# Kernel optimization log

Measured on AMD Instinct MI355X. Metric: run time of the kernel, lower is better.

Reference implementation:

```python
import jax, jax.numpy as jnp
import numpy as np

D = 512  # input_channels
K = 64   # centers_num


def setup_inputs() -> dict:
    key = jax.random.key(0)
    k1, k2, k3, k4 = jax.random.split(key, 4)
    inputs = jax.random.normal(k1, (32, D, 56, 56), dtype=jnp.float32)
    # conv 1x1 weight/bias (nn.Conv2d(input_channels, centers_num, (1,1)))
    conv_w = jax.random.normal(k2, (K, D), dtype=jnp.float32) * (1.0 / np.sqrt(D))
    conv_b = jax.random.normal(k3, (K,), dtype=jnp.float32) * 0.01
    # centers ~ U(-0.1, 0.1), shape [D, K]
    centers = jax.random.uniform(k4, (D, K), dtype=jnp.float32, minval=-0.1, maxval=0.1)
    return {"inputs": inputs, "conv_w": conv_w, "conv_b": conv_b, "centers": centers}


def reference(inputs, conv_w, conv_b, centers):
    B, d, H, W = inputs.shape
    N = H * W
    x = inputs.reshape(B, d, N)                      # [B,D,N]
    # 1x1 conv == per-pixel linear: logits [B,K,N]
    logits = jnp.einsum('kd,bdn->bkn', conv_w, x) + conv_b[None, :, None]
    alpha = jax.nn.softmax(logits, axis=1)           # softmax over K (dim=1)
    # vlad[b,d,k] = sum_n alpha[b,k,n] * (x[b,d,n] - centers[d,k])
    vlad = jnp.einsum('bkn,bdn->bdk', alpha, x) - centers[None] * alpha.sum(axis=2)[:, None, :]
    # intra-normalize over D (torch.norm default p=2, no eps)
    vlad = vlad / jnp.linalg.norm(vlad, axis=1, keepdims=True)
    vlad = vlad.reshape(B, d * K)
    vlad = vlad / jnp.linalg.norm(vlad, axis=1, keepdims=True)
    return vlad
```

## Files before the change

### kernel.cpp

```cpp
#include <hip/hip_runtime.h>
#include <math.h>


#define NN 3136
#define DD 512
#define KK 64
#define BB 32

typedef short bf16x8 __attribute__((ext_vector_type(8)));
typedef float f32x4  __attribute__((ext_vector_type(4)));

#define SEL_HI   0x05040100u
#define SEL_LO   0x07060302u
#define SEL_PACK 0x07060302u

union FragU { uint4 u; bf16x8 f; };

static __device__ inline bf16x8 frag4(unsigned a, unsigned b, unsigned c, unsigned d) {
    FragU x; x.u = make_uint4(a, b, c, d); return x.f;
}

static __device__ inline unsigned short bf16_rne(float f) {
    unsigned u = __float_as_uint(f);
    return (unsigned short)((u + 0x7FFFu + ((u >> 16) & 1u)) >> 16);
}

__global__ __launch_bounds__(256) void wprep_kernel(
    const float* __restrict__ w, unsigned short* __restrict__ wh,
    unsigned short* __restrict__ wl, float* __restrict__ asum,
    float* __restrict__ vlad)
{
    const int i = blockIdx.x * 256 + threadIdx.x;
    if (i < 32768) {
        float v = w[i];
        float hif = __uint_as_float(__float_as_uint(v) & 0xFFFF0000u);
        float lof = v - hif;
        wh[i] = (unsigned short)(__float_as_uint(v) >> 16);
        wl[i] = (unsigned short)(__float_as_uint(lof) >> 16);
    }
    *(float4*)&vlad[(size_t)i * 4] = make_float4(0.f, 0.f, 0.f, 0.f);
    if (i < 2048) asum[i] = 0.f;
}

__global__ __launch_bounds__(256) void logits_softmax_mfma(
    const float* __restrict__ x,
    const unsigned short* __restrict__ wh,
    const unsigned short* __restrict__ wl,
    const float* __restrict__ bias,
    unsigned short* __restrict__ alpha,
    float* __restrict__ asum)
{
    const int b  = blockIdx.y;
    const int n0 = blockIdx.x * 128;
    const int t  = threadIdx.x;
    const int lane = t & 63;
    const int wv   = t >> 6;
    const int c = lane & 15;
    const int q = lane >> 4;

    __shared__ __align__(16) unsigned xs[128][36];
    __shared__ __align__(16) unsigned short wsh[64][40];
    __shared__ __align__(16) unsigned short wsl[64][40];

    f32x4 acc[4][2];
    #pragma unroll
    for (int mt = 0; mt < 4; mt++)
        #pragma unroll
        for (int r = 0; r < 4; r++) {
            float bv = bias[mt * 16 + q * 4 + r];
            acc[mt][0][r] = bv; acc[mt][1][r] = bv;
        }

    const float* xb = x + (size_t)b * DD * NN;
    const int n4 = t & 31;
    const int dr = t >> 5;
    const int wrow = t >> 2, wc8 = t & 3;

    float xr[16];
    uint4 wrh, wrl;
    {
        #pragma unroll
        for (int j = 0; j < 4; j++) {
            int nn = n0 + n4 + 32 * j;
            if (nn > NN - 1) nn = NN - 1;
            #pragma unroll
            for (int p = 0; p < 4; p++)
                xr[j * 4 + p] = xb[(size_t)(dr * 4 + p) * NN + nn];
        }
        wrh = *(const uint4*)&wh[(size_t)wrow * DD + wc8 * 8];
        wrl = *(const uint4*)&wl[(size_t)wrow * DD + wc8 * 8];
    }

    for (int dc = 0; dc < 16; dc++) {
        uint4 xp[4];
        #pragma unroll
        for (int j = 0; j < 4; j++) {
            unsigned pk[4];
            #pragma unroll
            for (int p = 0; p < 4; p++) {
                float v = xr[j * 4 + p];
                float hif = __uint_as_float(__float_as_uint(v) & 0xFFFF0000u);
                float lof = v - hif;
                pk[p] = __builtin_amdgcn_perm(__float_as_uint(lof), __float_as_uint(v), SEL_PACK);
            }
            xp[j] = make_uint4(pk[0], pk[1], pk[2], pk[3]);
        }
        uint4 wch = wrh, wcl = wrl;

        if (dc < 15) {
            const int d0 = (dc + 1) * 32;
            #pragma unroll
            for (int j = 0; j < 4; j++) {
                int nn = n0 + n4 + 32 * j;
                if (nn > NN - 1) nn = NN - 1;
                #pragma unroll
                for (int p = 0; p < 4; p++)
                    xr[j * 4 + p] = xb[(size_t)(d0 + dr * 4 + p) * NN + nn];
            }
            wrh = *(const uint4*)&wh[(size_t)wrow * DD + d0 + wc8 * 8];
            wrl = *(const uint4*)&wl[(size_t)wrow * DD + d0 + wc8 * 8];
        }

        __syncthreads();
        #pragma unroll
        for (int j = 0; j < 4; j++)
            *(uint4*)&xs[n4 + 32 * j][dr * 4] = xp[j];
        *(uint4*)&wsh[wrow][wc8 * 8] = wch;
        *(uint4*)&wsl[wrow][wc8 * 8] = wcl;
        __syncthreads();

        bf16x8 ah[4], al[4], bh[2], bl[2];
        #pragma unroll
        for (int mt = 0; mt < 4; mt++) {
            ah[mt] = *(const bf16x8*)&wsh[mt * 16 + c][q * 8];
            al[mt] = *(const bf16x8*)&wsl[mt * 16 + c][q * 8];
        }
        #pragma unroll
        for (int nt = 0; nt < 2; nt++) {
            const int row = wv * 32 + nt * 16 + c;
            uint4 p0 = *(const uint4*)&xs[row][q * 8];
            uint4 p1 = *(const uint4*)&xs[row][q * 8 + 4];
            bh[nt] = frag4(__builtin_amdgcn_perm(p0.y, p0.x, SEL_HI),
                           __builtin_amdgcn_perm(p0.w, p0.z, SEL_HI),
                           __builtin_amdgcn_perm(p1.y, p1.x, SEL_HI),
                           __builtin_amdgcn_perm(p1.w, p1.z, SEL_HI));
            bl[nt] = frag4(__builtin_amdgcn_perm(p0.y, p0.x, SEL_LO),
                           __builtin_amdgcn_perm(p0.w, p0.z, SEL_LO),
                           __builtin_amdgcn_perm(p1.y, p1.x, SEL_LO),
                           __builtin_amdgcn_perm(p1.w, p1.z, SEL_LO));
        }
        #pragma unroll
        for (int mt = 0; mt < 4; mt++)
            #pragma unroll
            for (int nt = 0; nt < 2; nt++) {
                acc[mt][nt] = __builtin_amdgcn_mfma_f32_16x16x32_bf16(ah[mt], bh[nt], acc[mt][nt], 0, 0, 0);
                acc[mt][nt] = __builtin_amdgcn_mfma_f32_16x16x32_bf16(ah[mt], bl[nt], acc[mt][nt], 0, 0, 0);
                acc[mt][nt] = __builtin_amdgcn_mfma_f32_16x16x32_bf16(al[mt], bh[nt], acc[mt][nt], 0, 0, 0);
            }
    }

    unsigned short* ab = alpha + (size_t)b * KK * NN;
    float sa[4][4];
    #pragma unroll
    for (int mt = 0; mt < 4; mt++)
        #pragma unroll
        for (int r = 0; r < 4; r++) sa[mt][r] = 0.f;

    #pragma unroll
    for (int nt = 0; nt < 2; nt++) {
        float mx = -1e30f;
        #pragma unroll
        for (int mt = 0; mt < 4; mt++)
            #pragma unroll
            for (int r = 0; r < 4; r++) mx = fmaxf(mx, acc[mt][nt][r]);
        mx = fmaxf(mx, __shfl_xor(mx, 16));
        mx = fmaxf(mx, __shfl_xor(mx, 32));
        float s = 0.f;
        #pragma unroll
        for (int mt = 0; mt < 4; mt++)
            #pragma unroll
            for (int r = 0; r < 4; r++) {
                float e = __expf(acc[mt][nt][r] - mx);
                acc[mt][nt][r] = e; s += e;
            }
        s += __shfl_xor(s, 16);
        s += __shfl_xor(s, 32);
        const float rinv = 1.0f / s;
        const int pix = n0 + wv * 32 + nt * 16 + c;
        const bool ok = pix < NN;
        #pragma unroll
        for (int mt = 0; mt < 4; mt++)
            #pragma unroll
            for (int r = 0; r < 4; r++) {
                unsigned short ub = bf16_rne(acc[mt][nt][r] * rinv);
                if (ok) {
                    ab[(size_t)(mt * 16 + q * 4 + r) * NN + pix] = ub;
                    sa[mt][r] += __uint_as_float((unsigned)ub << 16);
                }
            }
    }
    #pragma unroll
    for (int off = 1; off <= 8; off <<= 1)
        #pragma unroll
        for (int mt = 0; mt < 4; mt++)
            #pragma unroll
            for (int r = 0; r < 4; r++)
                sa[mt][r] += __shfl_xor(sa[mt][r], off);
    if (c == 0) {
        #pragma unroll
        for (int mt = 0; mt < 4; mt++)
            #pragma unroll
            for (int r = 0; r < 4; r++)
                atomicAdd(&asum[b * KK + mt * 16 + q * 4 + r], sa[mt][r]);
    }
}

__global__ __launch_bounds__(256) void vlad_mfma(
    const float* __restrict__ x,
    const unsigned short* __restrict__ alpha,
    float* __restrict__ vlad)
{
    const int dtile = blockIdx.x;
    const int ns    = blockIdx.y;
    const int b     = blockIdx.z;
    const int t     = threadIdx.x;
    const int lane = t & 63;
    const int wv   = t >> 6;
    const int c = lane & 15;
    const int q = lane >> 4;

    __shared__ __align__(16) unsigned short xh[128][72];
    __shared__ __align__(16) unsigned short xl[128][72];
    __shared__ __align__(16) unsigned short as_[64][72];

    f32x4 acc[2][4];
    #pragma unroll
    for (int mt = 0; mt < 2; mt++)
        #pragma unroll
        for (int nt = 0; nt < 4; nt++)
            #pragma unroll
            for (int r = 0; r < 4; r++) acc[mt][nt][r] = 0.f;

    const float* xb = x + ((size_t)b * DD + dtile * 128) * NN;
    const int nq = t & 15, dr2 = t >> 4;
    const int arow = t >> 2, ac = t & 3;
    const int nchunk = 784;

    float4 xr[8];
    uint4  ar[2];
    {
        const int nb = ns * nchunk;
        #pragma unroll
        for (int p = 0; p < 8; p++)
            xr[p] = *(const float4*)&xb[(size_t)(dr2 + p * 16) * NN + nb + nq * 4];
        #pragma unroll
        for (int j = 0; j < 2; j++)
            ar[j] = *(const uint4*)&alpha[((size_t)b * KK + arow) * NN + nb + ac * 16 + j * 8];
    }

    for (int cc = 0; cc < 13; cc++) {
        uint2 ph[8], pl[8];
        #pragma unroll
        for (int p = 0; p < 8; p++) {
            float4 v = xr[p];
            unsigned ux = __float_as_uint(v.x), uy = __float_as_uint(v.y);
            unsigned uz = __float_as_uint(v.z), uw = __float_as_uint(v.w);
            ph[p].x = __builtin_amdgcn_perm(uy, ux, SEL_LO);
            ph[p].y = __builtin_amdgcn_perm(uw, uz, SEL_LO);
            float lx = v.x - __uint_as_float(ux & 0xFFFF0000u);
            float ly = v.y - __uint_as_float(uy & 0xFFFF0000u);
            float lz = v.z - __uint_as_float(uz & 0xFFFF0000u);
            float lw = v.w - __uint_as_float(uw & 0xFFFF0000u);
            pl[p].x = __builtin_amdgcn_perm(__float_as_uint(ly), __float_as_uint(lx), SEL_LO);
            pl[p].y = __builtin_amdgcn_perm(__float_as_uint(lw), __float_as_uint(lz), SEL_LO);
        }
        uint4 ac_[2] = { ar[0], ar[1] };

        if (cc < 12) {
            const int nb = ns * nchunk + (cc + 1) * 64;
            const int nvalid = min(64, nchunk - (cc + 1) * 64);
            #pragma unroll
            for (int p = 0; p < 8; p++) {
                xr[p] = make_float4(0.f, 0.f, 0.f, 0.f);
                if (nq * 4 < nvalid)
                    xr[p] = *(const float4*)&xb[(size_t)(dr2 + p * 16) * NN + nb + nq * 4];
            }
            #pragma unroll
            for (int j = 0; j < 2; j++) {
                const int col = ac * 16 + j * 8;
                ar[j] = make_uint4(0u, 0u, 0u, 0u);
                if (col < nvalid)
                    ar[j] = *(const uint4*)&alpha[((size_t)b * KK + arow) * NN + nb + col];
            }
        }

        __syncthreads();
        #pragma unroll
        for (int p = 0; p < 8; p++) {
            *(uint2*)&xh[dr2 + p * 16][nq * 4] = ph[p];
            *(uint2*)&xl[dr2 + p * 16][nq * 4] = pl[p];
        }
        #pragma unroll
        for (int j = 0; j < 2; j++)
            *(uint4*)&as_[arow][ac * 16 + j * 8] = ac_[j];
        __syncthreads();

        #pragma unroll
        for (int ks = 0; ks < 2; ks++) {
            const int colb = ks * 32 + q * 8;
            bf16x8 ah[2], al2[2], bh[4];
            #pragma unroll
            for (int mt = 0; mt < 2; mt++) {
                const int row = wv * 32 + mt * 16 + c;
                ah[mt]  = *(const bf16x8*)&xh[row][colb];
                al2[mt] = *(const bf16x8*)&xl[row][colb];
            }
            #pragma unroll
            for (int nt = 0; nt < 4; nt++)
                bh[nt] = *(const bf16x8*)&as_[nt * 16 + c][colb];
            #pragma unroll
            for (int mt = 0; mt < 2; mt++)
                #pragma unroll
                for (int nt = 0; nt < 4; nt++) {
                    acc[mt][nt] = __builtin_amdgcn_mfma_f32_16x16x32_bf16(ah[mt],  bh[nt], acc[mt][nt], 0, 0, 0);
                    acc[mt][nt] = __builtin_amdgcn_mfma_f32_16x16x32_bf16(al2[mt], bh[nt], acc[mt][nt], 0, 0, 0);
                }
        }
    }

    float* pv = vlad + ((size_t)b * DD + dtile * 128 + wv * 32) * KK;
    #pragma unroll
    for (int mt = 0; mt < 2; mt++)
        #pragma unroll
        for (int r = 0; r < 4; r++) {
            const int dl = mt * 16 + q * 4 + r;
            #pragma unroll
            for (int nt = 0; nt < 4; nt++)
                atomicAdd(&pv[(size_t)dl * KK + nt * 16 + c], acc[mt][nt][r]);
        }
}

__global__ __launch_bounds__(256) void combine_norm(
    const float* __restrict__ centers, const float* __restrict__ asum,
    float* __restrict__ vlad, float* __restrict__ psq)
{
    const int dchunk = blockIdx.x;
    const int b = blockIdx.y;
    const int t = threadIdx.x;
    const int k4 = (t & 15) * 4;
    const int dq = t >> 4;
    const float4 av = *(const float4*)&asum[b * KK + k4];
    float sqx = 0.f, sqy = 0.f, sqz = 0.f, sqw = 0.f;
    for (int i = 0; i < 8; i++) {
        const int d = dchunk * 128 + i * 16 + dq;
        const size_t idx = ((size_t)b * DD + d) * KK + k4;
        float4 p = *(const float4*)&vlad[idx];
        const float4 cv = *(const float4*)&centers[d * KK + k4];
        float vx = p.x - cv.x * av.x, vy = p.y - cv.y * av.y;
        float vz = p.z - cv.z * av.z, vw = p.w - cv.w * av.w;
        *(float4*)&vlad[idx] = make_float4(vx, vy, vz, vw);
        sqx = fmaf(vx, vx, sqx); sqy = fmaf(vy, vy, sqy);
        sqz = fmaf(vz, vz, sqz); sqw = fmaf(vw, vw, sqw);
    }
    __shared__ float red[16][64];
    red[dq][k4 + 0] = sqx; red[dq][k4 + 1] = sqy;
    red[dq][k4 + 2] = sqz; red[dq][k4 + 3] = sqw;
    __syncthreads();
    if (t < 64) {
        float s = 0.f;
        #pragma unroll
        for (int qq = 0; qq < 16; qq++) s += red[qq][t];
        psq[(b * 4 + dchunk) * 64 + t] = s;
    }
}

__global__ __launch_bounds__(256) void finalize_kernel(
    const float* __restrict__ psq, const float* __restrict__ vlad,
    float* __restrict__ out)
{
    const int dchunk = blockIdx.x;
    const int b = blockIdx.y;
    const int t = threadIdx.x;
    __shared__ float cn[64];
    if (t < 64) {
        float s = psq[b * 256 + t] + psq[b * 256 + 64 + t]
                + psq[b * 256 + 128 + t] + psq[b * 256 + 192 + t];
        cn[t] = 1.0f / (sqrtf(s) * 8.0f);
    }
    __syncthreads();
    const int k4 = (t & 15) * 4;
    const int dq = t >> 4;
    const float4 cv = *(const float4*)&cn[k4];
    #pragma unroll
    for (int i = 0; i < 8; i++) {
        const size_t idx = ((size_t)b * DD + dchunk * 128 + i * 16 + dq) * KK + k4;
        float4 v = *(const float4*)&vlad[idx];
        *(float4*)&out[idx] = make_float4(v.x * cv.x, v.y * cv.y, v.z * cv.z, v.w * cv.w);
    }
}

extern "C" void kernel_launch(void* const* d_in, const int* in_sizes, int n_in,
                              void* d_out, int out_size, void* d_ws, size_t ws_size,
                              hipStream_t stream) {
    const float* x       = (const float*)d_in[0];
    const float* conv_w  = (const float*)d_in[1];
    const float* conv_b  = (const float*)d_in[2];
    const float* centers = (const float*)d_in[3];
    float* out = (float*)d_out;

    unsigned short* wh    = (unsigned short*)d_ws;
    unsigned short* wl    = wh + 32768;
    unsigned short* alpha = wl + 32768;
    float* asum  = (float*)(alpha + (size_t)BB * KK * NN);
    float* vlad  = asum + 2048;
    float* psq   = vlad + 1048576;

    wprep_kernel       <<<dim3(1024),       dim3(256), 0, stream>>>(conv_w, wh, wl, asum, vlad);
    logits_softmax_mfma<<<dim3(25, BB),     dim3(256), 0, stream>>>(x, wh, wl, conv_b, alpha, asum);
    vlad_mfma          <<<dim3(4, 4, BB),   dim3(256), 0, stream>>>(x, alpha, vlad);
    combine_norm       <<<dim3(4, BB),      dim3(256), 0, stream>>>(centers, asum, vlad, psq);
    finalize_kernel    <<<dim3(4, BB),      dim3(256), 0, stream>>>(psq, vlad, out);
}
```

Before: 369.8 us.

## Fuse softmax-assignment and VLAD aggregation into one kernel via LDS alpha

Merges the logits/softmax kernel with the VLAD aggregation kernel. Each block keeps its bf16 alpha tile in shared memory and immediately multiplies it against the same pixel range of x, which it reloads from global memory (likely cache-resident) and splits into hi/lo bf16 on the fly. This removes the global alpha buffer write/read and one kernel launch. In exchange every block now atomically adds a full 512x64 partial into vlad, so atomic traffic grows substantially, and the per-lane x reads are narrower and less coalesced.

Measured after the change: 415.0 us. +12.2%, slower.

```diff
diff --git a/kernel.cpp b/kernel.cpp
--- a/kernel.cpp
+++ b/kernel.cpp
@@ -42,13 +42,13 @@
     if (i < 2048) asum[i] = 0.f;
 }
 
-__global__ __launch_bounds__(256) void logits_softmax_mfma(
+__global__ __launch_bounds__(256) void fused_vlad(
     const float* __restrict__ x,
     const unsigned short* __restrict__ wh,
     const unsigned short* __restrict__ wl,
     const float* __restrict__ bias,
-    unsigned short* __restrict__ alpha,
-    float* __restrict__ asum)
+    float* __restrict__ asum,
+    float* __restrict__ vlad)
 {
     const int b  = blockIdx.y;
     const int n0 = blockIdx.x * 128;
@@ -61,6 +61,7 @@
     __shared__ __align__(16) unsigned xs[128][36];
     __shared__ __align__(16) unsigned short wsh[64][40];
     __shared__ __align__(16) unsigned short wsl[64][40];
+    __shared__ __align__(16) unsigned short as_[64][136];
 
     f32x4 acc[4][2];
     #pragma unroll
@@ -159,7 +160,6 @@
             }
     }
 
-    unsigned short* ab = alpha + (size_t)b * KK * NN;
     float sa[4][4];
     #pragma unroll
     for (int mt = 0; mt < 4; mt++)
@@ -186,17 +186,16 @@
         s += __shfl_xor(s, 16);
         s += __shfl_xor(s, 32);
         const float rinv = 1.0f / s;
-        const int pix = n0 + wv * 32 + nt * 16 + c;
-        const bool ok = pix < NN;
+        const int nloc = wv * 32 + nt * 16 + c;
+        const bool ok = (n0 + nloc) < NN;
         #pragma unroll
         for (int mt = 0; mt < 4; mt++)
             #pragma unroll
             for (int r = 0; r < 4; r++) {
                 unsigned short ub = bf16_rne(acc[mt][nt][r] * rinv);
-                if (ok) {
-                    ab[(size_t)(mt * 16 + q * 4 + r) * NN + pix] = ub;
-                    sa[mt][r] += __uint_as_float((unsigned)ub << 16);
-                }
+                if (!ok) ub = 0;
+                as_[mt * 16 + q * 4 + r][nloc] = ub;
+                if (ok) sa[mt][r] += __uint_as_float((unsigned)ub << 16);
             }
     }
     #pragma unroll
@@ -213,131 +212,73 @@
             for (int r = 0; r < 4; r++)
                 atomicAdd(&asum[b * KK + mt * 16 + q * 4 + r], sa[mt][r]);
     }
-}
-
-__global__ __launch_bounds__(256) void vlad_mfma(
-    const float* __restrict__ x,
-    const unsigned short* __restrict__ alpha,
-    float* __restrict__ vlad)
-{
-    const int dtile = blockIdx.x;
-    const int ns    = blockIdx.y;
-    const int b     = blockIdx.z;
-    const int t     = threadIdx.x;
-    const int lane = t & 63;
-    const int wv   = t >> 6;
-    const int c = lane & 15;
-    const int q = lane >> 4;
-
-    __shared__ __align__(16) unsigned short xh[128][72];
-    __shared__ __align__(16) unsigned short xl[128][72];
-    __shared__ __align__(16) unsigned short as_[64][72];
-
-    f32x4 acc[2][4];
-    #pragma unroll
-    for (int mt = 0; mt < 2; mt++)
-        #pragma unroll
-        for (int nt = 0; nt < 4; nt++)
-            #pragma unroll
-            for (int r = 0; r < 4; r++) acc[mt][nt][r] = 0.f;
-
-    const float* xb = x + ((size_t)b * DD + dtile * 128) * NN;
-    const int nq = t & 15, dr2 = t >> 4;
-    const int arow = t >> 2, ac = t & 3;
-    const int nchunk = 784;
-
-    float4 xr[8];
-    uint4  ar[2];
-    {
-        const int nb = ns * nchunk;
-        #pragma unroll
-        for (int p = 0; p < 8; p++)
-            xr[p] = *(const float4*)&xb[(size_t)(dr2 + p * 16) * NN + nb + nq * 4];
-        #pragma unroll
-        for (int j = 0; j < 2; j++)
-            ar[j] = *(const uint4*)&alpha[((size_t)b * KK + arow) * NN + nb + ac * 16 + j * 8];
-    }
-
-    for (int cc = 0; cc < 13; cc++) {
-        uint2 ph[8], pl[8];
-        #pragma unroll
-        for (int p = 0; p < 8; p++) {
-            float4 v = xr[p];
-            unsigned ux = __float_as_uint(v.x), uy = __float_as_uint(v.y);
-            unsigned uz = __float_as_uint(v.z), uw = __float_as_uint(v.w);
-            ph[p].x = __builtin_amdgcn_perm(uy, ux, SEL_LO);
-            ph[p].y = __builtin_amdgcn_perm(uw, uz, SEL_LO);
-            float lx = v.x - __uint_as_float(ux & 0xFFFF0000u);
-            float ly = v.y - __uint_as_float(uy & 0xFFFF0000u);
-            float lz = v.z - __uint_as_float(uz & 0xFFFF0000u);
-            float lw = v.w - __uint_as_float(uw & 0xFFFF0000u);
-            pl[p].x = __builtin_amdgcn_perm(__float_as_uint(ly), __float_as_uint(lx), SEL_LO);
-            pl[p].y = __builtin_amdgcn_perm(__float_as_uint(lw), __float_as_uint(lz), SEL_LO);
-        }
-        uint4 ac_[2] = { ar[0], ar[1] };
-
-        if (cc < 12) {
-            const int nb = ns * nchunk + (cc + 1) * 64;
-            const int nvalid = min(64, nchunk - (cc + 1) * 64);
-            #pragma unroll
-            for (int p = 0; p < 8; p++) {
-                xr[p] = make_float4(0.f, 0.f, 0.f, 0.f);
-                if (nq * 4 < nvalid)
-                    xr[p] = *(const float4*)&xb[(size_t)(dr2 + p * 16) * NN + nb + nq * 4];
-            }
-            #pragma unroll
-            for (int j = 0; j < 2; j++) {
-                const int col = ac * 16 + j * 8;
-                ar[j] = make_uint4(0u, 0u, 0u, 0u);
-                if (col < nvalid)
-                    ar[j] = *(const uint4*)&alpha[((size_t)b * KK + arow) * NN + nb + col];
-            }
-        }
-
-        __syncthreads();
-        #pragma unroll
-        for (int p = 0; p < 8; p++) {
-            *(uint2*)&xh[dr2 + p * 16][nq * 4] = ph[p];
-            *(uint2*)&xl[dr2 + p * 16][nq * 4] = pl[p];
-        }
-        #pragma unroll
-        for (int j = 0; j < 2; j++)
-            *(uint4*)&as_[arow][ac * 16 + j * 8] = ac_[j];
-        __syncthreads();
-
-        #pragma unroll
-        for (int ks = 0; ks < 2; ks++) {
-            const int colb = ks * 32 + q * 8;
-            bf16x8 ah[2], al2[2], bh[4];
-            #pragma unroll
-            for (int mt = 0; mt < 2; mt++) {
-                const int row = wv * 32 + mt * 16 + c;
-                ah[mt]  = *(const bf16x8*)&xh[row][colb];
-                al2[mt] = *(const bf16x8*)&xl[row][colb];
-            }
-            #pragma unroll
-            for (int nt = 0; nt < 4; nt++)
-                bh[nt] = *(const bf16x8*)&as_[nt * 16 + c][colb];
-            #pragma unroll
-            for (int mt = 0; mt < 2; mt++)
+
+    __syncthreads();
+
+    const float* xw = x + ((size_t)b * DD + wv * 128) * NN;
+    float* pvb = vlad + ((size_t)b * DD + wv * 128) * KK;
+
+    #pragma unroll
+    for (int dh = 0; dh < 2; dh++) {
+        f32x4 acc2[4][4];
+        #pragma unroll
+        for (int dt = 0; dt < 4; dt++)
+            #pragma unroll
+            for (int kt = 0; kt < 4; kt++)
                 #pragma unroll
-                for (int nt = 0; nt < 4; nt++) {
-                    acc[mt][nt] = __builtin_amdgcn_mfma_f32_16x16x32_bf16(ah[mt],  bh[nt], acc[mt][nt], 0, 0, 0);
-                    acc[mt][nt] = __builtin_amdgcn_mfma_f32_16x16x32_bf16(al2[mt], bh[nt], acc[mt][nt], 0, 0, 0);
+                for (int r = 0; r < 4; r++) acc2[dt][kt][r] = 0.f;
+
+        #pragma unroll
+        for (int ns = 0; ns < 4; ns++) {
+            bf16x8 bfr[4];
+            #pragma unroll
+            for (int kt = 0; kt < 4; kt++)
+                bfr[kt] = *(const bf16x8*)&as_[kt * 16 + c][ns * 32 + q * 8];
+            int nn = n0 + ns * 32 + q * 8;
+            if (nn > NN - 8) nn = NN - 8;
+            #pragma unroll
+            for (int dt = 0; dt < 4; dt++) {
+                const size_t ro = (size_t)(dh * 64 + dt * 16 + c) * NN;
+                const float4 va = *(const float4*)&xw[ro + nn];
+                const float4 vb2 = *(const float4*)&xw[ro + nn + 4];
+                unsigned ux = __float_as_uint(va.x),  uy = __float_as_uint(va.y);
+                unsigned uz = __float_as_uint(va.z),  uw = __float_as_uint(va.w);
+                unsigned vx = __float_as_uint(vb2.x), vy = __float_as_uint(vb2.y);
+                unsigned vz = __float_as_uint(vb2.z), vw = __float_as_uint(vb2.w);
+                bf16x8 ah = frag4(__builtin_amdgcn_perm(uy, ux, SEL_LO),
+                                  __builtin_amdgcn_perm(uw, uz, SEL_LO),
+                                  __builtin_amdgcn_perm(vy, vx, SEL_LO),
+                                  __builtin_amdgcn_perm(vw, vz, SEL_LO));
+                float lax = va.x - __uint_as_float(ux & 0xFFFF0000u);
+                float lay = va.y - __uint_as_float(uy & 0xFFFF0000u);
+                float laz = va.z - __uint_as_float(uz & 0xFFFF0000u);
+                float law = va.w - __uint_as_float(uw & 0xFFFF0000u);
+                float lbx = vb2.x - __uint_as_float(vx & 0xFFFF0000u);
+                float lby = vb2.y - __uint_as_float(vy & 0xFFFF0000u);
+                float lbz = vb2.z - __uint_as_float(vz & 0xFFFF0000u);
+                float lbw = vb2.w - __uint_as_float(vw & 0xFFFF0000u);
+                bf16x8 al2 = frag4(
+                    __builtin_amdgcn_perm(__float_as_uint(lay), __float_as_uint(lax), SEL_LO),
+                    __builtin_amdgcn_perm(__float_as_uint(law), __float_as_uint(laz), SEL_LO),
+                    __builtin_amdgcn_perm(__float_as_uint(lby), __float_as_uint(lbx), SEL_LO),
+                    __builtin_amdgcn_perm(__float_as_uint(lbw), __float_as_uint(lbz), SEL_LO));
+                #pragma unroll
+                for (int kt = 0; kt < 4; kt++) {
+                    acc2[dt][kt] = __builtin_amdgcn_mfma_f32_16x16x32_bf16(ah,  bfr[kt], acc2[dt][kt], 0, 0, 0);
+                    acc2[dt][kt] = __builtin_amdgcn_mfma_f32_16x16x32_bf16(al2, bfr[kt], acc2[dt][kt], 0, 0, 0);
                 }
-        }
-    }
-
-    float* pv = vlad + ((size_t)b * DD + dtile * 128 + wv * 32) * KK;
-    #pragma unroll
-    for (int mt = 0; mt < 2; mt++)
-        #pragma unroll
-        for (int r = 0; r < 4; r++) {
-            const int dl = mt * 16 + q * 4 + r;
-            #pragma unroll
-            for (int nt = 0; nt < 4; nt++)
-                atomicAdd(&pv[(size_t)dl * KK + nt * 16 + c], acc[mt][nt][r]);
-        }
+            }
+        }
+        #pragma unroll
+        for (int dt = 0; dt < 4; dt++)
+            #pragma unroll
+            for (int r = 0; r < 4; r++) {
+                const size_t dl = (size_t)(dh * 64 + dt * 16 + q * 4 + r) * KK;
+                #pragma unroll
+                for (int kt = 0; kt < 4; kt++)
+                    atomicAdd(&pvb[dl + kt * 16 + c], acc2[dt][kt][r]);
+            }
+    }
 }
 
 __global__ __launch_bounds__(256) void combine_norm(
@@ -408,16 +349,14 @@
     const float* centers = (const float*)d_in[3];
     float* out = (float*)d_out;
 
-    unsigned short* wh    = (unsigned short*)d_ws;
-    unsigned short* wl    = wh + 32768;
-    unsigned short* alpha = wl + 32768;
-    float* asum  = (float*)(alpha + (size_t)BB * KK * NN);
-    float* vlad  = asum + 2048;
-    float* psq   = vlad + 1048576;
-
-    wprep_kernel       <<<dim3(1024),       dim3(256), 0, stream>>>(conv_w, wh, wl, asum, vlad);
-    logits_softmax_mfma<<<dim3(25, BB),     dim3(256), 0, stream>>>(x, wh, wl, conv_b, alpha, asum);
-    vlad_mfma          <<<dim3(4, 4, BB),   dim3(256), 0, stream>>>(x, alpha, vlad);
-    combine_norm       <<<dim3(4, BB),      dim3(256), 0, stream>>>(centers, asum, vlad, psq);
-    finalize_kernel    <<<dim3(4, BB),      dim3(256), 0, stream>>>(psq, vlad, out);
-}
+    unsigned short* wh = (unsigned short*)d_ws;
+    unsigned short* wl = wh + 32768;
+    float* asum = (float*)(wl + 32768);
+    float* vlad = asum + 2048;
+    float* psq  = vlad + 1048576;
+
+    wprep_kernel   <<<dim3(1024),    dim3(256), 0, stream>>>(conv_w, wh, wl, asum, vlad);
+    fused_vlad     <<<dim3(25, BB),  dim3(256), 0, stream>>>(x, wh, wl, conv_b, asum, vlad);
+    combine_norm   <<<dim3(4, BB),   dim3(256), 0, stream>>>(centers, asum, vlad, psq);
+    finalize_kernel<<<dim3(4, BB),   dim3(256), 0, stream>>>(psq, vlad, out);
+}
```
